# Kernel optimization log

Measured on AMD Instinct MI355X. Metric: run time of the kernel, lower is better.

## Reference

```python
import jax, jax.numpy as jnp
import numpy as np

B, C, N = 8, 256, 2048
H = max(1, C // 8)  # hidden = in_channels // 8 = 32


def setup_inputs() -> dict:
    key = jax.random.key(0)
    ks = jax.random.split(key, 7)
    s = 0.05
    return {
        "x": jax.random.normal(ks[0], (B, C, N), dtype=jnp.float32),
        "wq": jax.random.normal(ks[1], (H, C), dtype=jnp.float32) * s,
        "bq": jax.random.normal(ks[2], (H,), dtype=jnp.float32) * s,
        "wk": jax.random.normal(ks[3], (H, C), dtype=jnp.float32) * s,
        "bk": jax.random.normal(ks[4], (H,), dtype=jnp.float32) * s,
        "wv": jax.random.normal(ks[5], (C, C), dtype=jnp.float32) * s,
        "bv": jax.random.normal(ks[6], (C,), dtype=jnp.float32) * s,
    }


def reference(x, wq, bq, wk, bk, wv, bv):
    # 1x1 Conv1d == per-position linear: weight [out, in]
    q = jnp.einsum('bcn,hc->bnh', x, wq) + bq                  # [B, N, H] (already permuted)
    k = jnp.einsum('bcn,hc->bhn', x, wk) + bk[None, :, None]   # [B, H, N]
    v = jnp.einsum('bcn,dc->bdn', x, wv) + bv[None, :, None]   # [B, C, N]
    energy = jnp.einsum('bnh,bhm->bnm', q, k)                  # [B, N, N] (no scaling, as in source)
    weights = jax.nn.softmax(energy, axis=-1)                  # softmax over last dim
    # out = bmm(value, weights^T): out[b,c,i] = sum_j v[b,c,j] * weights[b,i,j]
    out = jnp.einsum('bcj,bij->bci', v, weights)               # [B, C, N]
    return out + x
```

## Files before the change

kernel.cpp:

```cpp
#include <hip/hip_runtime.h>
#include <hip/hip_bf16.h>
#include <cstdint>
#include <cstddef>

#define B_ 8
#define C_ 256
#define N_ 2048
#define H_ 32
#define VP_ 2064
#define NT_ (N_ / 64)

typedef __bf16 bf8 __attribute__((ext_vector_type(8)));
typedef __bf16 bf4 __attribute__((ext_vector_type(4)));
typedef float f4 __attribute__((ext_vector_type(4)));
typedef float f16v __attribute__((ext_vector_type(16)));

__device__ inline void gload_lds16(const void* g, void* l) {
  __builtin_amdgcn_global_load_lds(
      (const __attribute__((address_space(1))) unsigned int*)g,
      (__attribute__((address_space(3))) unsigned int*)l, 16, 0, 0);
}

__global__ __launch_bounds__(256) void pack_kernel(
    const float* __restrict__ wq, const float* __restrict__ wk,
    const float* __restrict__ wv, const float* __restrict__ bq,
    const float* __restrict__ bk, const float* __restrict__ bv,
    __hip_bfloat16* __restrict__ wpk, float* __restrict__ bpk) {
  int r = blockIdx.x, c = threadIdx.x;
  float v;
  if (r < 256)      v = wv[r * 256 + c];
  else if (r < 288) v = wq[(r - 256) * 256 + c];
  else              v = wk[(r - 288) * 256 + c];
  wpk[r * 256 + c] = __float2bfloat16(v);
  if (c == 0) bpk[r] = (r < 256) ? bv[r] : (r < 288 ? bq[r - 256] : bk[r - 288]);
}

__global__ __launch_bounds__(256) void proj_kernel(
    const float* __restrict__ x, const __hip_bfloat16* __restrict__ wpk,
    const float* __restrict__ bpk, __hip_bfloat16* __restrict__ vbf,
    __hip_bfloat16* __restrict__ qkb) {
  __shared__ __attribute__((aligned(16))) __hip_bfloat16 As[2][320 * 32];
  int tid = threadIdx.x, wv = tid >> 6, lane = tid & 63;
  int b = blockIdx.y;
  int n0 = blockIdx.x * 32;
  int fcol = lane & 15, hi4 = lane >> 4;
  int grow = lane >> 2, gc = (lane & 3) * 8;
  const float* xb = x + (size_t)b * C_ * N_;

#pragma unroll
  for (int g = 0; g < 5; ++g)
    gload_lds16(wpk + (size_t)(wv * 80 + g * 16 + grow) * 256 + gc,
                &As[0][(wv * 80 + g * 16) * 32]);
  float xr[2][8];
#pragma unroll
  for (int j = 0; j < 2; ++j)
#pragma unroll
    for (int e = 0; e < 8; ++e)
      xr[j][e] = xb[(size_t)(hi4 * 8 + e) * N_ + n0 + j * 16 + fcol];

  f4 acc[5][2] = {};
  for (int t = 0; t < 8; ++t) {
    int buf = t & 1;
    __syncthreads();
    if (t < 7) {
      int k1 = (t + 1) * 32;
#pragma unroll
      for (int g = 0; g < 5; ++g)
        gload_lds16(wpk + (size_t)(wv * 80 + g * 16 + grow) * 256 + k1 + gc,
                    &As[buf ^ 1][(wv * 80 + g * 16) * 32]);
    }
    bf8 bfr[2];
#pragma unroll
    for (int j = 0; j < 2; ++j)
#pragma unroll
      for (int e = 0; e < 8; ++e) bfr[j][e] = (__bf16)xr[j][e];
    if (t < 7) {
      int k1 = (t + 1) * 32;
#pragma unroll
      for (int j = 0; j < 2; ++j)
#pragma unroll
        for (int e = 0; e < 8; ++e)
          xr[j][e] = xb[(size_t)(k1 + hi4 * 8 + e) * N_ + n0 + j * 16 + fcol];
    }
#pragma unroll
    for (int s = 0; s < 5; ++s) {
      bf8 af = *(const bf8*)&As[buf][(wv * 80 + s * 16 + fcol) * 32 + hi4 * 8];
      acc[s][0] = __builtin_amdgcn_mfma_f32_16x16x32_bf16(af, bfr[0], acc[s][0], 0, 0, 0);
      acc[s][1] = __builtin_amdgcn_mfma_f32_16x16x32_bf16(af, bfr[1], acc[s][1], 0, 0, 0);
    }
  }
  int rq = hi4 * 4;
#pragma unroll
  for (int s = 0; s < 5; ++s)
#pragma unroll
    for (int r = 0; r < 4; ++r) {
      int m = wv * 80 + s * 16 + rq + r;
      float bias = bpk[m];
#pragma unroll
      for (int j = 0; j < 2; ++j) {
        int n = n0 + j * 16 + fcol;
        float val = acc[s][j][r] + bias;
        if (m < 256)
          vbf[((size_t)b * C_ + m) * VP_ + n] = __float2bfloat16(val);
        else
          qkb[((size_t)b * N_ + n) * 64 + (m - 256)] = __float2bfloat16(val);
      }
    }
}

__global__ __launch_bounds__(256, 2) void fused_attn(
    const __hip_bfloat16* __restrict__ qk,
    const __hip_bfloat16* __restrict__ vbf,
    const float* __restrict__ x, float* __restrict__ out) {
  __shared__ __attribute__((aligned(16))) __hip_bfloat16 pS[2][64][88];
  __shared__ float lSp[2][64];
  int tid = threadIdx.x;
  int wv = tid >> 6, lane = tid & 63;
  int l31 = lane & 31, hi = lane >> 5;
  int ws_i = wv >> 1, ws_j = wv & 1;
  int blk = blockIdx.x;
  int b = blk & 7;
  int rest = blk >> 3;
  int c0 = (rest & 1) * 128;
  int i0 = (rest >> 1) * 64;

  const __hip_bfloat16* qkB = qk + (size_t)b * N_ * 64;
  const __hip_bfloat16* qp = qkB + (size_t)(i0 + ws_i * 32 + l31) * 64 + hi * 8;
  bf8 qf0 = *(const bf8*)qp;
  bf8 qf1 = *(const bf8*)(qp + 16);
  const __hip_bfloat16* kp = qkB + (size_t)(ws_j * 32 + l31) * 64 + 32 + hi * 8;
  bf8 kf0 = *(const bf8*)kp;
  bf8 kf1 = *(const bf8*)(kp + 16);
  const __hip_bfloat16* vR =
      vbf + ((size_t)b * C_ + c0 + wv * 32 + l31) * VP_ + hi * 8;
  bf8 vf0 = *(const bf8*)vR;
  bf8 vf1 = *(const bf8*)(vR + 16);
  bf8 vf2 = *(const bf8*)(vR + 32);
  bf8 vf3 = *(const bf8*)(vR + 48);

  f16v acc0 = {}, acc1 = {};
  float lp0 = 0.f, lp1 = 0.f;

#define PV_STEP(KB, VA)                                                       \
  {                                                                           \
    const __hip_bfloat16* pr = &pS[buf][l31][(KB) * 16 + hi * 8];             \
    bf8 pf0 = *(const bf8*)pr;                                                \
    bf8 pf1 = *(const bf8*)(pr + 32 * 88);                                    \
    acc0 = __builtin_amdgcn_mfma_f32_32x32x16_bf16(VA, pf0, acc0, 0, 0, 0);   \
    acc1 = __builtin_amdgcn_mfma_f32_32x32x16_bf16(VA, pf1, acc1, 0, 0, 0);   \
  }

  for (int t = 0; t < NT_; ++t) {
    int buf = t & 1;
    f16v s = {};
    s = __builtin_amdgcn_mfma_f32_32x32x16_bf16(kf0, qf0, s, 0, 0, 0);
    s = __builtin_amdgcn_mfma_f32_32x32x16_bf16(kf1, qf1, s, 0, 0, 0);
    bf8 kn0, kn1, vn0, vn1, vn2, vn3;
    if (t + 1 < NT_) {
      const __hip_bfloat16* kpn = kp + (size_t)(t + 1) * 64 * 64;
      kn0 = *(const bf8*)kpn;
      kn1 = *(const bf8*)(kpn + 16);
      const __hip_bfloat16* vpn = vR + (t + 1) * 64;
      vn0 = *(const bf8*)vpn;
      vn1 = *(const bf8*)(vpn + 16);
      vn2 = *(const bf8*)(vpn + 32);
      vn3 = *(const bf8*)(vpn + 48);
    }
#pragma unroll
    for (int r = 0; r < 16; ++r) s[r] = __expf(s[r]);
#pragma unroll
    for (int r = 0; r < 16; r += 2) { lp0 += s[r]; lp1 += s[r + 1]; }
    __hip_bfloat16* pw = &pS[buf][ws_i * 32 + l31][ws_j * 32 + 4 * hi];
#pragma unroll
    for (int q = 0; q < 4; ++q) {
      bf4 tb;
      tb[0] = (__bf16)s[4 * q + 0];
      tb[1] = (__bf16)s[4 * q + 1];
      tb[2] = (__bf16)s[4 * q + 2];
      tb[3] = (__bf16)s[4 * q + 3];
      *(bf4*)(pw + 8 * q) = tb;
    }
    asm volatile("s_waitcnt lgkmcnt(0)" ::: "memory");
    __builtin_amdgcn_s_barrier();
    asm volatile("" ::: "memory");
    __builtin_amdgcn_s_setprio(1);
    PV_STEP(0, vf0)
    PV_STEP(1, vf1)
    PV_STEP(2, vf2)
    PV_STEP(3, vf3)
    __builtin_amdgcn_s_setprio(0);
    if (t + 1 < NT_) {
      kf0 = kn0; kf1 = kn1;
      vf0 = vn0; vf1 = vn1; vf2 = vn2; vf3 = vn3;
    }
  }
#undef PV_STEP

  float lp = lp0 + lp1;
  lp += __shfl_xor(lp, 32);
  if (lane < 32) lSp[ws_j][ws_i * 32 + l31] = lp;
  __syncthreads();
  float linv0 = 1.0f / (lSp[0][l31] + lSp[1][l31]);
  float linv1 = 1.0f / (lSp[0][32 + l31] + lSp[1][32 + l31]);

  const float* xr = x + (size_t)b * C_ * N_;
  float* op = out + (size_t)b * C_ * N_;
#pragma unroll
  for (int r = 0; r < 16; ++r) {
    int crow = (r & 3) + 8 * (r >> 2) + 4 * hi;
    size_t o = (size_t)(c0 + wv * 32 + crow) * N_ + i0 + l31;
    op[o] = acc0[r] * linv0 + xr[o];
    op[o + 32] = acc1[r] * linv1 + xr[o + 32];
  }
}

extern "C" void kernel_launch(void* const* d_in, const int* in_sizes, int n_in,
                              void* d_out, int out_size, void* d_ws, size_t ws_size,
                              hipStream_t stream) {
  const float* x  = (const float*)d_in[0];
  const float* wq = (const float*)d_in[1];
  const float* bq = (const float*)d_in[2];
  const float* wk = (const float*)d_in[3];
  const float* bk = (const float*)d_in[4];
  const float* wv = (const float*)d_in[5];
  const float* bv = (const float*)d_in[6];
  float* out = (float*)d_out;

  char* ws = (char*)d_ws;
  __hip_bfloat16* qkb = (__hip_bfloat16*)ws;
  __hip_bfloat16* vbf = (__hip_bfloat16*)(ws + (2u << 20));
  __hip_bfloat16* wpk = (__hip_bfloat16*)(ws + 10551296u);
  float*          bpk = (float*)(ws + 10551296u + 163840u);

  pack_kernel<<<dim3(320), 256, 0, stream>>>(wq, wk, wv, bq, bk, bv, wpk, bpk);
  proj_kernel<<<dim3(N_ / 32, B_), 256, 0, stream>>>(x, wpk, bpk, vbf, qkb);
  fused_attn<<<dim3(512), 256, 0, stream>>>(qkb, vbf, x, out);
}
```

Measured before the change: 127.5 us.

## Split attention across more blocks, fold log2e into Q, unroll double-buffered loop

The attention kernel now has each block handle 64 output channels instead of 128, so the grid doubles to 1024 blocks and each wave keeps one 32x32 accumulator instead of two. Launch bounds rise to 4 blocks per CU to raise occupancy. The Q weights and bias are pre-scaled by log2(e), so the softmax can use the raw exp2 instruction. The main loop is unrolled by two with ping-pong register sets for K/V prefetch, removing the per-iteration register copies. In exchange, the QK^T MFMA and exp work are now repeated four times per row tile instead of twice, and K is reloaded by twice as many blocks.

```diff
diff --git a/kernel.cpp b/kernel.cpp
--- a/kernel.cpp
+++ b/kernel.cpp
@@ -26,13 +26,14 @@
     const float* __restrict__ wv, const float* __restrict__ bq,
     const float* __restrict__ bk, const float* __restrict__ bv,
     __hip_bfloat16* __restrict__ wpk, float* __restrict__ bpk) {
+  const float L2E = 1.44269504088896f;
   int r = blockIdx.x, c = threadIdx.x;
   float v;
   if (r < 256)      v = wv[r * 256 + c];
-  else if (r < 288) v = wq[(r - 256) * 256 + c];
+  else if (r < 288) v = wq[(r - 256) * 256 + c] * L2E;
   else              v = wk[(r - 288) * 256 + c];
   wpk[r * 256 + c] = __float2bfloat16(v);
-  if (c == 0) bpk[r] = (r < 256) ? bv[r] : (r < 288 ? bq[r - 256] : bk[r - 288]);
+  if (c == 0) bpk[r] = (r < 256) ? bv[r] : (r < 288 ? bq[r - 256] * L2E : bk[r - 288]);
 }
 
 __global__ __launch_bounds__(256) void proj_kernel(
@@ -108,109 +109,108 @@
     }
 }
 
-__global__ __launch_bounds__(256, 2) void fused_attn(
+#define ATTN_BODY(T, BUF, CK0, CK1, CV0, CV1, CV2, CV3,                        \
+                  NK0, NK1, NV0, NV1, NV2, NV3)                                \
+  {                                                                            \
+    int tn_ = (T) + 1 < NT_ ? (T) + 1 : (T);                                   \
+    const __hip_bfloat16* kpn_ = kp + (size_t)tn_ * 64 * 64;                   \
+    NK0 = *(const bf8*)kpn_;                                                   \
+    NK1 = *(const bf8*)(kpn_ + 16);                                            \
+    const __hip_bfloat16* vpn_ = vR + tn_ * 64;                                \
+    NV0 = *(const bf8*)vpn_;                                                   \
+    NV1 = *(const bf8*)(vpn_ + 16);                                            \
+    NV2 = *(const bf8*)(vpn_ + 32);                                            \
+    NV3 = *(const bf8*)(vpn_ + 48);                                            \
+    f16v s = {};                                                               \
+    s = __builtin_amdgcn_mfma_f32_32x32x16_bf16(CK0, qf0, s, 0, 0, 0);         \
+    s = __builtin_amdgcn_mfma_f32_32x32x16_bf16(CK1, qf1, s, 0, 0, 0);         \
+    _Pragma("unroll")                                                          \
+    for (int r = 0; r < 16; ++r) s[r] = __builtin_amdgcn_exp2f(s[r]);          \
+    _Pragma("unroll")                                                          \
+    for (int r = 0; r < 16; r += 2) { lp0 += s[r]; lp1 += s[r + 1]; }          \
+    __hip_bfloat16* pw_ = &pS[BUF][iw * 32 + l31][jw * 32 + 4 * hi];           \
+    _Pragma("unroll")                                                          \
+    for (int q = 0; q < 4; ++q) {                                              \
+      bf4 tb_;                                                                 \
+      tb_[0] = (__bf16)s[4 * q + 0];                                           \
+      tb_[1] = (__bf16)s[4 * q + 1];                                           \
+      tb_[2] = (__bf16)s[4 * q + 2];                                           \
+      tb_[3] = (__bf16)s[4 * q + 3];                                           \
+      *(bf4*)(pw_ + 8 * q) = tb_;                                              \
+    }                                                                          \
+    asm volatile("s_waitcnt lgkmcnt(0)" ::: "memory");                         \
+    __builtin_amdgcn_s_barrier();                                              \
+    const __hip_bfloat16* pr_ = &pS[BUF][iw * 32 + l31][hi * 8];               \
+    __builtin_amdgcn_s_setprio(1);                                             \
+    {                                                                          \
+      bf8 pf0_ = *(const bf8*)(pr_ + 0);                                       \
+      acc = __builtin_amdgcn_mfma_f32_32x32x16_bf16(CV0, pf0_, acc, 0, 0, 0);  \
+      bf8 pf1_ = *(const bf8*)(pr_ + 16);                                      \
+      acc = __builtin_amdgcn_mfma_f32_32x32x16_bf16(CV1, pf1_, acc, 0, 0, 0);  \
+      bf8 pf2_ = *(const bf8*)(pr_ + 32);                                      \
+      acc = __builtin_amdgcn_mfma_f32_32x32x16_bf16(CV2, pf2_, acc, 0, 0, 0);  \
+      bf8 pf3_ = *(const bf8*)(pr_ + 48);                                      \
+      acc = __builtin_amdgcn_mfma_f32_32x32x16_bf16(CV3, pf3_, acc, 0, 0, 0);  \
+    }                                                                          \
+    __builtin_amdgcn_s_setprio(0);                                             \
+  }
+
+__global__ __launch_bounds__(256, 4) void fused_attn(
     const __hip_bfloat16* __restrict__ qk,
     const __hip_bfloat16* __restrict__ vbf,
     const float* __restrict__ x, float* __restrict__ out) {
   __shared__ __attribute__((aligned(16))) __hip_bfloat16 pS[2][64][88];
   __shared__ float lSp[2][64];
   int tid = threadIdx.x;
-  int wv = tid >> 6, lane = tid & 63;
+  int w = tid >> 6, lane = tid & 63;
   int l31 = lane & 31, hi = lane >> 5;
-  int ws_i = wv >> 1, ws_j = wv & 1;
+  int jw = w & 1, iw = w >> 1;
   int blk = blockIdx.x;
   int b = blk & 7;
   int rest = blk >> 3;
-  int c0 = (rest & 1) * 128;
-  int i0 = (rest >> 1) * 64;
+  int cs = rest & 3;
+  int i0 = (rest >> 2) * 64;
 
   const __hip_bfloat16* qkB = qk + (size_t)b * N_ * 64;
-  const __hip_bfloat16* qp = qkB + (size_t)(i0 + ws_i * 32 + l31) * 64 + hi * 8;
+  const __hip_bfloat16* qp = qkB + (size_t)(i0 + iw * 32 + l31) * 64 + hi * 8;
   bf8 qf0 = *(const bf8*)qp;
   bf8 qf1 = *(const bf8*)(qp + 16);
-  const __hip_bfloat16* kp = qkB + (size_t)(ws_j * 32 + l31) * 64 + 32 + hi * 8;
-  bf8 kf0 = *(const bf8*)kp;
-  bf8 kf1 = *(const bf8*)(kp + 16);
+  const __hip_bfloat16* kp = qkB + (size_t)(jw * 32 + l31) * 64 + 32 + hi * 8;
   const __hip_bfloat16* vR =
-      vbf + ((size_t)b * C_ + c0 + wv * 32 + l31) * VP_ + hi * 8;
-  bf8 vf0 = *(const bf8*)vR;
-  bf8 vf1 = *(const bf8*)(vR + 16);
-  bf8 vf2 = *(const bf8*)(vR + 32);
-  bf8 vf3 = *(const bf8*)(vR + 48);
-
-  f16v acc0 = {}, acc1 = {};
+      vbf + ((size_t)b * C_ + cs * 64 + jw * 32 + l31) * VP_ + hi * 8;
+
+  bf8 kA0 = *(const bf8*)kp;
+  bf8 kA1 = *(const bf8*)(kp + 16);
+  bf8 vA0 = *(const bf8*)vR;
+  bf8 vA1 = *(const bf8*)(vR + 16);
+  bf8 vA2 = *(const bf8*)(vR + 32);
+  bf8 vA3 = *(const bf8*)(vR + 48);
+  bf8 kB0, kB1, vB0, vB1, vB2, vB3;
+
+  f16v acc = {};
   float lp0 = 0.f, lp1 = 0.f;
 
-#define PV_STEP(KB, VA)                                                       \
-  {                                                                           \
-    const __hip_bfloat16* pr = &pS[buf][l31][(KB) * 16 + hi * 8];             \
-    bf8 pf0 = *(const bf8*)pr;                                                \
-    bf8 pf1 = *(const bf8*)(pr + 32 * 88);                                    \
-    acc0 = __builtin_amdgcn_mfma_f32_32x32x16_bf16(VA, pf0, acc0, 0, 0, 0);   \
-    acc1 = __builtin_amdgcn_mfma_f32_32x32x16_bf16(VA, pf1, acc1, 0, 0, 0);   \
-  }
-
-  for (int t = 0; t < NT_; ++t) {
-    int buf = t & 1;
-    f16v s = {};
-    s = __builtin_amdgcn_mfma_f32_32x32x16_bf16(kf0, qf0, s, 0, 0, 0);
-    s = __builtin_amdgcn_mfma_f32_32x32x16_bf16(kf1, qf1, s, 0, 0, 0);
-    bf8 kn0, kn1, vn0, vn1, vn2, vn3;
-    if (t + 1 < NT_) {
-      const __hip_bfloat16* kpn = kp + (size_t)(t + 1) * 64 * 64;
-      kn0 = *(const bf8*)kpn;
-      kn1 = *(const bf8*)(kpn + 16);
-      const __hip_bfloat16* vpn = vR + (t + 1) * 64;
-      vn0 = *(const bf8*)vpn;
-      vn1 = *(const bf8*)(vpn + 16);
-      vn2 = *(const bf8*)(vpn + 32);
-      vn3 = *(const bf8*)(vpn + 48);
-    }
-#pragma unroll
-    for (int r = 0; r < 16; ++r) s[r] = __expf(s[r]);
-#pragma unroll
-    for (int r = 0; r < 16; r += 2) { lp0 += s[r]; lp1 += s[r + 1]; }
-    __hip_bfloat16* pw = &pS[buf][ws_i * 32 + l31][ws_j * 32 + 4 * hi];
-#pragma unroll
-    for (int q = 0; q < 4; ++q) {
-      bf4 tb;
-      tb[0] = (__bf16)s[4 * q + 0];
-      tb[1] = (__bf16)s[4 * q + 1];
-      tb[2] = (__bf16)s[4 * q + 2];
-      tb[3] = (__bf16)s[4 * q + 3];
-      *(bf4*)(pw + 8 * q) = tb;
-    }
-    asm volatile("s_waitcnt lgkmcnt(0)" ::: "memory");
-    __builtin_amdgcn_s_barrier();
-    asm volatile("" ::: "memory");
-    __builtin_amdgcn_s_setprio(1);
-    PV_STEP(0, vf0)
-    PV_STEP(1, vf1)
-    PV_STEP(2, vf2)
-    PV_STEP(3, vf3)
-    __builtin_amdgcn_s_setprio(0);
-    if (t + 1 < NT_) {
-      kf0 = kn0; kf1 = kn1;
-      vf0 = vn0; vf1 = vn1; vf2 = vn2; vf3 = vn3;
-    }
-  }
-#undef PV_STEP
+  for (int tt = 0; tt < NT_; tt += 2) {
+    ATTN_BODY(tt, 0, kA0, kA1, vA0, vA1, vA2, vA3,
+              kB0, kB1, vB0, vB1, vB2, vB3)
+    ATTN_BODY(tt + 1, 1, kB0, kB1, vB0, vB1, vB2, vB3,
+              kA0, kA1, vA0, vA1, vA2, vA3)
+  }
 
   float lp = lp0 + lp1;
   lp += __shfl_xor(lp, 32);
-  if (lane < 32) lSp[ws_j][ws_i * 32 + l31] = lp;
+  if (lane < 32) lSp[jw][iw * 32 + l31] = lp;
   __syncthreads();
-  float linv0 = 1.0f / (lSp[0][l31] + lSp[1][l31]);
-  float linv1 = 1.0f / (lSp[0][32 + l31] + lSp[1][32 + l31]);
+  float linv = 1.0f / (lSp[0][iw * 32 + l31] + lSp[1][iw * 32 + l31]);
 
   const float* xr = x + (size_t)b * C_ * N_;
   float* op = out + (size_t)b * C_ * N_;
+  int i = i0 + iw * 32 + l31;
 #pragma unroll
   for (int r = 0; r < 16; ++r) {
     int crow = (r & 3) + 8 * (r >> 2) + 4 * hi;
-    size_t o = (size_t)(c0 + wv * 32 + crow) * N_ + i0 + l31;
-    op[o] = acc0[r] * linv0 + xr[o];
-    op[o + 32] = acc1[r] * linv1 + xr[o + 32];
+    size_t o = (size_t)(cs * 64 + jw * 32 + crow) * N_ + i;
+    op[o] = acc[r] * linv + xr[o];
   }
 }
 
@@ -234,5 +234,5 @@
 
   pack_kernel<<<dim3(320), 256, 0, stream>>>(wq, wk, wv, bq, bk, bv, wpk, bpk);
   proj_kernel<<<dim3(N_ / 32, B_), 256, 0, stream>>>(x, wpk, bpk, vbf, qkb);
-  fused_attn<<<dim3(512), 256, 0, stream>>>(qkb, vbf, x, out);
-}
+  fused_attn<<<dim3(1024), 256, 0, stream>>>(qkb, vbf, x, out);
+}
```

Result: slower. 151.7 us (+19.0%).

## Software-pipeline attention loop: overlap next QK^T/exp with current PV MFMAs

Applied to the files above, without the earlier changes.

Restructures the fused attention loop so each iteration computes the P·V MFMAs for tile t while computing the QK^T scores, exp and LDS write for tile t+1. K/V fragments are prefetched two tiles ahead, and the loop is unrolled by two with ping-pong register sets. It also folds log2(e) into the packed Q weights and bias, so the kernel can use the hardware exp2 instruction instead of __expf. This is meant to hide exp/LDS latency and barrier stalls behind matrix work, at the cost of more registers, which could hurt occupancy or spill.

```diff
diff --git a/kernel.cpp b/kernel.cpp
--- a/kernel.cpp
+++ b/kernel.cpp
@@ -26,13 +26,14 @@
     const float* __restrict__ wv, const float* __restrict__ bq,
     const float* __restrict__ bk, const float* __restrict__ bv,
     __hip_bfloat16* __restrict__ wpk, float* __restrict__ bpk) {
+  const float L2E = 1.44269504088896f;
   int r = blockIdx.x, c = threadIdx.x;
   float v;
   if (r < 256)      v = wv[r * 256 + c];
-  else if (r < 288) v = wq[(r - 256) * 256 + c];
+  else if (r < 288) v = wq[(r - 256) * 256 + c] * L2E;
   else              v = wk[(r - 288) * 256 + c];
   wpk[r * 256 + c] = __float2bfloat16(v);
-  if (c == 0) bpk[r] = (r < 256) ? bv[r] : (r < 288 ? bq[r - 256] : bk[r - 288]);
+  if (c == 0) bpk[r] = (r < 256) ? bv[r] : (r < 288 ? bq[r - 256] * L2E : bk[r - 288]);
 }
 
 __global__ __launch_bounds__(256) void proj_kernel(
@@ -107,6 +108,68 @@
       }
     }
 }
+
+#define ATTN_BODY(T, BUF, KC0, KC1, KN0, KN1, VC0, VC1, VC2, VC3)              \
+  {                                                                            \
+    const __hip_bfloat16* pr_ = &pS[BUF][l31][hi * 8];                         \
+    bf8 pf0_ = *(const bf8*)(pr_ + 0);                                         \
+    bf8 pf4_ = *(const bf8*)(pr_ + 32 * 88);                                   \
+    bf8 pf1_ = *(const bf8*)(pr_ + 16);                                        \
+    bf8 pf5_ = *(const bf8*)(pr_ + 32 * 88 + 16);                              \
+    bf8 pf2_ = *(const bf8*)(pr_ + 32);                                        \
+    bf8 pf6_ = *(const bf8*)(pr_ + 32 * 88 + 32);                              \
+    bf8 pf3_ = *(const bf8*)(pr_ + 48);                                        \
+    bf8 pf7_ = *(const bf8*)(pr_ + 32 * 88 + 48);                              \
+    f16v s_ = {};                                                              \
+    if ((T) + 1 < NT_) {                                                       \
+      s_ = __builtin_amdgcn_mfma_f32_32x32x16_bf16(KC0, qf0, s_, 0, 0, 0);     \
+      s_ = __builtin_amdgcn_mfma_f32_32x32x16_bf16(KC1, qf1, s_, 0, 0, 0);     \
+    }                                                                          \
+    {                                                                          \
+      int tn_ = (T) + 2 < NT_ ? (T) + 2 : NT_ - 1;                             \
+      const __hip_bfloat16* kpn_ = kp + (size_t)tn_ * 64 * 64;                 \
+      KN0 = *(const bf8*)kpn_;                                                 \
+      KN1 = *(const bf8*)(kpn_ + 16);                                          \
+    }                                                                          \
+    __builtin_amdgcn_s_setprio(1);                                             \
+    acc0 = __builtin_amdgcn_mfma_f32_32x32x16_bf16(VC0, pf0_, acc0, 0, 0, 0);  \
+    acc1 = __builtin_amdgcn_mfma_f32_32x32x16_bf16(VC0, pf4_, acc1, 0, 0, 0);  \
+    acc0 = __builtin_amdgcn_mfma_f32_32x32x16_bf16(VC1, pf1_, acc0, 0, 0, 0);  \
+    acc1 = __builtin_amdgcn_mfma_f32_32x32x16_bf16(VC1, pf5_, acc1, 0, 0, 0);  \
+    acc0 = __builtin_amdgcn_mfma_f32_32x32x16_bf16(VC2, pf2_, acc0, 0, 0, 0);  \
+    acc1 = __builtin_amdgcn_mfma_f32_32x32x16_bf16(VC2, pf6_, acc1, 0, 0, 0);  \
+    acc0 = __builtin_amdgcn_mfma_f32_32x32x16_bf16(VC3, pf3_, acc0, 0, 0, 0);  \
+    acc1 = __builtin_amdgcn_mfma_f32_32x32x16_bf16(VC3, pf7_, acc1, 0, 0, 0);  \
+    __builtin_amdgcn_s_setprio(0);                                             \
+    {                                                                          \
+      int tn_ = (T) + 2 < NT_ ? (T) + 2 : NT_ - 1;                             \
+      const __hip_bfloat16* vpn_ = vR + tn_ * 64;                              \
+      VC0 = *(const bf8*)vpn_;                                                 \
+      VC1 = *(const bf8*)(vpn_ + 16);                                          \
+      VC2 = *(const bf8*)(vpn_ + 32);                                          \
+      VC3 = *(const bf8*)(vpn_ + 48);                                          \
+    }                                                                          \
+    if ((T) + 1 < NT_) {                                                       \
+      _Pragma("unroll")                                                        \
+      for (int r = 0; r < 16; ++r) s_[r] = __builtin_amdgcn_exp2f(s_[r]);      \
+      _Pragma("unroll")                                                        \
+      for (int r = 0; r < 16; r += 2) { lp0 += s_[r]; lp1 += s_[r + 1]; }      \
+      __hip_bfloat16* pw_ = &pS[(BUF) ^ 1][ws_i * 32 + l31][ws_j * 32 + 4 * hi];\
+      _Pragma("unroll")                                                        \
+      for (int q = 0; q < 4; ++q) {                                            \
+        bf4 tb_;                                                               \
+        tb_[0] = (__bf16)s_[4 * q + 0];                                        \
+        tb_[1] = (__bf16)s_[4 * q + 1];                                        \
+        tb_[2] = (__bf16)s_[4 * q + 2];                                        \
+        tb_[3] = (__bf16)s_[4 * q + 3];                                        \
+        *(bf4*)(pw_ + 8 * q) = tb_;                                            \
+      }                                                                        \
+      asm volatile("s_waitcnt lgkmcnt(0)" ::: "memory");                       \
+      __builtin_amdgcn_sched_barrier(0);                                       \
+      __builtin_amdgcn_s_barrier();                                            \
+      __builtin_amdgcn_sched_barrier(0);                                       \
+    }                                                                          \
+  }
 
 __global__ __launch_bounds__(256, 2) void fused_attn(
     const __hip_bfloat16* __restrict__ qk,
@@ -129,72 +192,55 @@
   bf8 qf0 = *(const bf8*)qp;
   bf8 qf1 = *(const bf8*)(qp + 16);
   const __hip_bfloat16* kp = qkB + (size_t)(ws_j * 32 + l31) * 64 + 32 + hi * 8;
-  bf8 kf0 = *(const bf8*)kp;
-  bf8 kf1 = *(const bf8*)(kp + 16);
   const __hip_bfloat16* vR =
       vbf + ((size_t)b * C_ + c0 + wv * 32 + l31) * VP_ + hi * 8;
-  bf8 vf0 = *(const bf8*)vR;
-  bf8 vf1 = *(const bf8*)(vR + 16);
-  bf8 vf2 = *(const bf8*)(vR + 32);
-  bf8 vf3 = *(const bf8*)(vR + 48);
+
+  bf8 k00 = *(const bf8*)kp;
+  bf8 k01 = *(const bf8*)(kp + 16);
+  bf8 kO0 = *(const bf8*)(kp + 64 * 64);
+  bf8 kO1 = *(const bf8*)(kp + 64 * 64 + 16);
+  bf8 kE0, kE1;
+  bf8 vE0 = *(const bf8*)vR;
+  bf8 vE1 = *(const bf8*)(vR + 16);
+  bf8 vE2 = *(const bf8*)(vR + 32);
+  bf8 vE3 = *(const bf8*)(vR + 48);
+  bf8 vO0 = *(const bf8*)(vR + 64);
+  bf8 vO1 = *(const bf8*)(vR + 64 + 16);
+  bf8 vO2 = *(const bf8*)(vR + 64 + 32);
+  bf8 vO3 = *(const bf8*)(vR + 64 + 48);
 
   f16v acc0 = {}, acc1 = {};
   float lp0 = 0.f, lp1 = 0.f;
 
-#define PV_STEP(KB, VA)                                                       \
-  {                                                                           \
-    const __hip_bfloat16* pr = &pS[buf][l31][(KB) * 16 + hi * 8];             \
-    bf8 pf0 = *(const bf8*)pr;                                                \
-    bf8 pf1 = *(const bf8*)(pr + 32 * 88);                                    \
-    acc0 = __builtin_amdgcn_mfma_f32_32x32x16_bf16(VA, pf0, acc0, 0, 0, 0);   \
-    acc1 = __builtin_amdgcn_mfma_f32_32x32x16_bf16(VA, pf1, acc1, 0, 0, 0);   \
-  }
-
-  for (int t = 0; t < NT_; ++t) {
-    int buf = t & 1;
-    f16v s = {};
-    s = __builtin_amdgcn_mfma_f32_32x32x16_bf16(kf0, qf0, s, 0, 0, 0);
-    s = __builtin_amdgcn_mfma_f32_32x32x16_bf16(kf1, qf1, s, 0, 0, 0);
-    bf8 kn0, kn1, vn0, vn1, vn2, vn3;
-    if (t + 1 < NT_) {
-      const __hip_bfloat16* kpn = kp + (size_t)(t + 1) * 64 * 64;
-      kn0 = *(const bf8*)kpn;
-      kn1 = *(const bf8*)(kpn + 16);
-      const __hip_bfloat16* vpn = vR + (t + 1) * 64;
-      vn0 = *(const bf8*)vpn;
-      vn1 = *(const bf8*)(vpn + 16);
-      vn2 = *(const bf8*)(vpn + 32);
-      vn3 = *(const bf8*)(vpn + 48);
-    }
-#pragma unroll
-    for (int r = 0; r < 16; ++r) s[r] = __expf(s[r]);
-#pragma unroll
-    for (int r = 0; r < 16; r += 2) { lp0 += s[r]; lp1 += s[r + 1]; }
-    __hip_bfloat16* pw = &pS[buf][ws_i * 32 + l31][ws_j * 32 + 4 * hi];
+  {
+    f16v s_ = {};
+    s_ = __builtin_amdgcn_mfma_f32_32x32x16_bf16(k00, qf0, s_, 0, 0, 0);
+    s_ = __builtin_amdgcn_mfma_f32_32x32x16_bf16(k01, qf1, s_, 0, 0, 0);
+#pragma unroll
+    for (int r = 0; r < 16; ++r) s_[r] = __builtin_amdgcn_exp2f(s_[r]);
+#pragma unroll
+    for (int r = 0; r < 16; r += 2) { lp0 += s_[r]; lp1 += s_[r + 1]; }
+    __hip_bfloat16* pw_ = &pS[0][ws_i * 32 + l31][ws_j * 32 + 4 * hi];
 #pragma unroll
     for (int q = 0; q < 4; ++q) {
-      bf4 tb;
-      tb[0] = (__bf16)s[4 * q + 0];
-      tb[1] = (__bf16)s[4 * q + 1];
-      tb[2] = (__bf16)s[4 * q + 2];
-      tb[3] = (__bf16)s[4 * q + 3];
-      *(bf4*)(pw + 8 * q) = tb;
+      bf4 tb_;
+      tb_[0] = (__bf16)s_[4 * q + 0];
+      tb_[1] = (__bf16)s_[4 * q + 1];
+      tb_[2] = (__bf16)s_[4 * q + 2];
+      tb_[3] = (__bf16)s_[4 * q + 3];
+      *(bf4*)(pw_ + 8 * q) = tb_;
     }
     asm volatile("s_waitcnt lgkmcnt(0)" ::: "memory");
+    __builtin_amdgcn_sched_barrier(0);
     __builtin_amdgcn_s_barrier();
-    asm volatile("" ::: "memory");
-    __builtin_amdgcn_s_setprio(1);
-    PV_STEP(0, vf0)
-    PV_STEP(1, vf1)
-    PV_STEP(2, vf2)
-    PV_STEP(3, vf3)
-    __builtin_amdgcn_s_setprio(0);
-    if (t + 1 < NT_) {
-      kf0 = kn0; kf1 = kn1;
-      vf0 = vn0; vf1 = vn1; vf2 = vn2; vf3 = vn3;
-    }
-  }
-#undef PV_STEP
+    __builtin_amdgcn_sched_barrier(0);
+  }
+
+  for (int tt = 0; tt < NT_; tt += 2) {
+    ATTN_BODY(tt,     0, kO0, kO1, kE0, kE1, vE0, vE1, vE2, vE3)
+    ATTN_BODY(tt + 1, 1, kE0, kE1, kO0, kO1, vO0, vO1, vO2, vO3)
+  }
+#undef ATTN_BODY
 
   float lp = lp0 + lp1;
   lp += __shfl_xor(lp, 32);
```

Measured after the change: 128.2 us. No clear change (+0.6%).
